# Optimization experiments

Hardware: AMD Instinct MI355X
Metric: run time of the kernel (lower is better)

The kernel has to match this reference:

```python
import jax, jax.numpy as jnp
import numpy as np

N_HEAD = 16


def setup_inputs() -> dict:
    key = jax.random.key(0)
    ks = jax.random.split(key, 4)
    B, S, E = 1, 4096, 1024
    x = jax.random.normal(ks[0], (B, S, E), dtype=jnp.float32)
    # causal mask: True where attention is DISALLOWED (upper triangle)
    masked_matrix = ~jnp.tril(jnp.ones((S, S), dtype=bool))[None, None]
    Wqkv = jax.random.normal(ks[1], (E, 3 * E), dtype=jnp.float32) * (1.0 / np.sqrt(E))
    bqkv = jnp.zeros((3 * E,), dtype=jnp.float32)
    Wp = jax.random.normal(ks[2], (E, E), dtype=jnp.float32) * (1.0 / np.sqrt(E))
    bp = jnp.zeros((E,), dtype=jnp.float32)
    return {"x": x, "masked_matrix": masked_matrix, "Wqkv": Wqkv, "bqkv": bqkv,
            "Wp": Wp, "bp": bp}


def reference(x, masked_matrix, Wqkv, bqkv, Wp, bp):
    B, S, E = x.shape
    H = N_HEAD
    D = E // H
    qkv = x @ Wqkv + bqkv                        # [B,S,3E]
    q, k, v = jnp.split(qkv, 3, axis=-1)
    q = q.reshape(B, S, H, D).transpose(0, 2, 1, 3)  # [B,H,S,D]
    k = k.reshape(B, S, H, D).transpose(0, 2, 1, 3)
    v = v.reshape(B, S, H, D).transpose(0, 2, 1, 3)
    # NOTE: source applies NO 1/sqrt(D) scaling — kept faithful.
    att = jnp.einsum('bhqd,bhkd->bhqk', q, k)    # [B,H,S,S]
    att = jnp.where(masked_matrix, jnp.float32(-jnp.inf), att)
    att = jax.nn.softmax(att, axis=-1)
    res = jnp.einsum('bhqk,bhkd->bhqd', att, v)  # [B,H,S,D]
    res = res.transpose(0, 2, 1, 3).reshape(B, S, E)
    return res @ Wp + bp
```

## Files before the change

### kernel.cpp

```cpp
#include <hip/hip_runtime.h>
#include <hip/hip_bf16.h>
#include <math.h>

#define S_LEN 4096
#define EMB   1024
#define NHEAD 16
#define HDIM  64

typedef __attribute__((ext_vector_type(8))) _Float16 half8;
typedef __attribute__((ext_vector_type(4))) _Float16 half4;
typedef __attribute__((ext_vector_type(4))) float float4_t;

#define GLOBAL_AS(p) ((const __attribute__((address_space(1))) void*)(p))
#define LDS_AS(p)    ((__attribute__((address_space(3))) void*)(p))

#define LOG2E 1.4426950408889634f

__global__ __launch_bounds__(256) void convert_f16(
    const float* __restrict__ in, _Float16* __restrict__ out)
{
    const int i = blockIdx.x * 256 + threadIdx.x;
    const float4_t v = ((const float4_t*)in)[i];
    half4 h;
#pragma unroll
    for (int j = 0; j < 4; ++j) h[j] = (_Float16)v[j];
    ((half4*)out)[i] = h;
}

__global__ __launch_bounds__(256) void transpose_f16(
    const float* __restrict__ in, _Float16* __restrict__ out, int R, int C)
{
    __shared__ float t[64][65];
    const int r0 = blockIdx.y * 64, c0 = blockIdx.x * 64;
    for (int i = threadIdx.x; i < 64 * 64; i += 256) {
        int r = i >> 6, c = i & 63;
        t[r][c] = in[(size_t)(r0 + r) * C + c0 + c];
    }
    __syncthreads();
    for (int i = threadIdx.x; i < 64 * 64; i += 256) {
        int c = i >> 6, r = i & 63;
        out[(size_t)(c0 + c) * R + r0 + r] = (_Float16)t[r][c];
    }
}

__global__ __launch_bounds__(256) void gemm_qkv(
    const _Float16* __restrict__ Ag, const _Float16* __restrict__ Bg,
    const float* __restrict__ bias,
    _Float16* __restrict__ qk, _Float16* __restrict__ vt, int K)
{
    constexpr int BK = 32;
    __shared__ _Float16 Ah[128 * BK];
    __shared__ _Float16 Bh[128 * BK];

    const int tid = threadIdx.x;
    const int wave = tid >> 6, lane = tid & 63;
    const int l16 = lane & 15, quad = lane >> 4;
    const int wr = wave >> 1, wc = wave & 1;
    const int row0 = blockIdx.y * 128, col0 = blockIdx.x * 128;
    const int lrow = lane >> 2, lc8 = (lane & 3) * 8;

    float4_t acc[4][4];
#pragma unroll
    for (int i = 0; i < 4; ++i)
#pragma unroll
        for (int j = 0; j < 4; ++j) acc[i][j] = (float4_t){0.f, 0.f, 0.f, 0.f};

    for (int k0 = 0; k0 < K; k0 += BK) {
        __syncthreads();
#pragma unroll
        for (int i = 0; i < 2; ++i) {
            const int ar = i * 64 + wave * 16;
            __builtin_amdgcn_global_load_lds(
                GLOBAL_AS(Ag + (size_t)(row0 + ar + lrow) * K + k0 + lc8),
                LDS_AS(&Ah[ar * BK]), 16, 0, 0);
            __builtin_amdgcn_global_load_lds(
                GLOBAL_AS(Bg + (size_t)(col0 + ar + lrow) * K + k0 + lc8),
                LDS_AS(&Bh[ar * BK]), 16, 0, 0);
        }
        __syncthreads();

        half8 af[4], bfr[4];
#pragma unroll
        for (int t = 0; t < 4; ++t) {
            af[t]  = *(const half8*)&Ah[(wr * 64 + t * 16 + l16) * BK + quad * 8];
            bfr[t] = *(const half8*)&Bh[(wc * 64 + t * 16 + l16) * BK + quad * 8];
        }
#pragma unroll
        for (int i = 0; i < 4; ++i)
#pragma unroll
            for (int j = 0; j < 4; ++j)
                acc[i][j] = __builtin_amdgcn_mfma_f32_16x16x32_f16(af[i], bfr[j], acc[i][j], 0, 0, 0);
    }

#pragma unroll
    for (int i = 0; i < 4; ++i) {
#pragma unroll
        for (int j = 0; j < 4; ++j) {
            const int colb = col0 + wc * 64 + j * 16 + l16;
            const float bv = bias[colb];
#pragma unroll
            for (int r = 0; r < 4; ++r) {
                const int row = row0 + wr * 64 + i * 16 + quad * 4 + r;
                float val = acc[i][j][r] + bv;
                if (colb < 2048) {
                    if (colb >= 1024) val *= LOG2E;
                    qk[(size_t)row * 2048 + colb] = (_Float16)val;
                } else {
                    vt[(size_t)(colb - 2048) * 4096 + row] = (_Float16)val;
                }
            }
        }
    }
}

__global__ __launch_bounds__(256) void gemm_out(
    const _Float16* __restrict__ Ag, const _Float16* __restrict__ Bg,
    const float* __restrict__ bias, float* __restrict__ C, int N, int K)
{
    constexpr int BK = 32;
    __shared__ _Float16 Ah[128 * BK];
    __shared__ _Float16 Bh[128 * BK];

    const int tid = threadIdx.x;
    const int wave = tid >> 6, lane = tid & 63;
    const int l16 = lane & 15, quad = lane >> 4;
    const int wr = wave >> 1, wc = wave & 1;
    const int row0 = blockIdx.y * 128, col0 = blockIdx.x * 128;
    const int lrow = lane >> 2, lc8 = (lane & 3) * 8;

    float4_t acc[4][4];
#pragma unroll
    for (int i = 0; i < 4; ++i)
#pragma unroll
        for (int j = 0; j < 4; ++j) acc[i][j] = (float4_t){0.f, 0.f, 0.f, 0.f};

    for (int k0 = 0; k0 < K; k0 += BK) {
        __syncthreads();
#pragma unroll
        for (int i = 0; i < 2; ++i) {
            const int ar = i * 64 + wave * 16;
            __builtin_amdgcn_global_load_lds(
                GLOBAL_AS(Ag + (size_t)(row0 + ar + lrow) * K + k0 + lc8),
                LDS_AS(&Ah[ar * BK]), 16, 0, 0);
            __builtin_amdgcn_global_load_lds(
                GLOBAL_AS(Bg + (size_t)(col0 + ar + lrow) * K + k0 + lc8),
                LDS_AS(&Bh[ar * BK]), 16, 0, 0);
        }
        __syncthreads();

        half8 af[4], bfr[4];
#pragma unroll
        for (int t = 0; t < 4; ++t) {
            af[t]  = *(const half8*)&Ah[(wr * 64 + t * 16 + l16) * BK + quad * 8];
            bfr[t] = *(const half8*)&Bh[(wc * 64 + t * 16 + l16) * BK + quad * 8];
        }
#pragma unroll
        for (int i = 0; i < 4; ++i)
#pragma unroll
            for (int j = 0; j < 4; ++j)
                acc[i][j] = __builtin_amdgcn_mfma_f32_16x16x32_f16(af[i], bfr[j], acc[i][j], 0, 0, 0);
    }

#pragma unroll
    for (int i = 0; i < 4; ++i) {
#pragma unroll
        for (int j = 0; j < 4; ++j) {
            const int colb = col0 + wc * 64 + j * 16 + l16;
            const float bv = bias[colb];
#pragma unroll
            for (int r = 0; r < 4; ++r) {
                const int row = row0 + wr * 64 + i * 16 + quad * 4 + r;
                C[(size_t)row * N + colb] = acc[i][j][r] + bv;
            }
        }
    }
}

__global__ __launch_bounds__(128, 2) void flash_attn_f16(
    const _Float16* __restrict__ qk, const _Float16* __restrict__ v_t,
    _Float16* __restrict__ resh)
{
    __shared__ __align__(16) _Float16 Ks[64][72];
    __shared__ __align__(16) _Float16 Vt[64][72];
    __shared__ __align__(16) _Float16 Pb[2][16][72];

    const int bid  = blockIdx.x;
    const int h    = (bid & 7) * 2 + ((bid >> 3) & 1);
    const int pair = bid >> 4;
    const int tid  = threadIdx.x;
    const int wave = tid >> 6;
    const int lane = tid & 63;
    const int l16  = lane & 15;
    const int quad = lane >> 4;
    const int srow = tid >> 3;
    const int sc8  = (tid & 7) * 8;

    for (int half = 0; half < 2; ++half) {
        const int tile = half ? 127 - pair : pair;
        const int q0   = tile * 32 + wave * 16;
        const int kb_last = (tile >> 1) * 64;

        const size_t qoff = (size_t)(q0 + l16) * 2048 + h * HDIM + quad * 8;
        half8 qf0 = *(const half8*)(qk + qoff);
        half8 qf1 = *(const half8*)(qk + qoff + 32);

        float4_t o[4];
#pragma unroll
        for (int c = 0; c < 4; ++c) o[c] = (float4_t){0.f, 0.f, 0.f, 0.f};
        float m_r = -INFINITY, l_r = 0.f;

        half8 pf_k[4], pf_v[4];
#pragma unroll
        for (int p = 0; p < 4; ++p) {
            const int r = srow + p * 16;
            pf_k[p] = *(const half8*)(qk + (size_t)r * 2048 + 1024 + h * HDIM + sc8);
            pf_v[p] = *(const half8*)(v_t + (size_t)(h * HDIM + r) * 4096 + sc8);
        }

        for (int kb = 0; kb <= kb_last; kb += 64) {
            __syncthreads();
#pragma unroll
            for (int p = 0; p < 4; ++p) {
                const int r = srow + p * 16;
                *(half8*)&Ks[r][sc8] = pf_k[p];
                *(half8*)&Vt[r][sc8] = pf_v[p];
            }
            __syncthreads();

            if (kb < kb_last) {
                const int kn = kb + 64;
#pragma unroll
                for (int p = 0; p < 4; ++p) {
                    const int r = srow + p * 16;
                    pf_k[p] = *(const half8*)(qk + (size_t)(kn + r) * 2048 + 1024 + h * HDIM + sc8);
                    pf_v[p] = *(const half8*)(v_t + (size_t)(h * HDIM + r) * 4096 + kn + sc8);
                }
            }

            if (kb > q0 + 15) continue;

            float4_t s[4];
#pragma unroll
            for (int t = 0; t < 4; ++t) {
                half8 a0 = *(const half8*)&Ks[t * 16 + l16][quad * 8];
                half8 a1 = *(const half8*)&Ks[t * 16 + l16][32 + quad * 8];
                float4_t a = (float4_t){0.f, 0.f, 0.f, 0.f};
                a = __builtin_amdgcn_mfma_f32_16x16x32_f16(a0, qf0, a, 0, 0, 0);
                a = __builtin_amdgcn_mfma_f32_16x16x32_f16(a1, qf1, a, 0, 0, 0);
                s[t] = a;
            }

            if (kb + 63 > q0) {
                const int qg = q0 + l16;
#pragma unroll
                for (int t = 0; t < 4; ++t)
#pragma unroll
                    for (int r = 0; r < 4; ++r) {
                        const int key = kb + t * 16 + quad * 4 + r;
                        if (key > qg) s[t][r] = -INFINITY;
                    }
            }

            float mx = s[0][0];
#pragma unroll
            for (int t = 0; t < 4; ++t)
#pragma unroll
                for (int r = 0; r < 4; ++r) mx = fmaxf(mx, s[t][r]);
            mx = fmaxf(mx, __shfl_xor(mx, 16));
            mx = fmaxf(mx, __shfl_xor(mx, 32));
            const float mnew  = fmaxf(m_r, mx);
            const float alpha = __builtin_amdgcn_exp2f(m_r - mnew);

            float p[4][4];
            float sum = 0.f;
#pragma unroll
            for (int t = 0; t < 4; ++t)
#pragma unroll
                for (int r = 0; r < 4; ++r) {
                    p[t][r] = __builtin_amdgcn_exp2f(s[t][r] - mnew);
                    sum += p[t][r];
                }
            sum += __shfl_xor(sum, 16);
            sum += __shfl_xor(sum, 32);
            l_r = l_r * alpha + sum;
            m_r = mnew;
#pragma unroll
            for (int ct = 0; ct < 4; ++ct)
#pragma unroll
                for (int r = 0; r < 4; ++r) o[ct][r] *= alpha;

#pragma unroll
            for (int t = 0; t < 4; ++t) {
                half4 w;
#pragma unroll
                for (int r = 0; r < 4; ++r) w[r] = (_Float16)p[t][r];
                *(half4*)&Pb[wave][l16][t * 16 + quad * 4] = w;
            }
            half8 pb0 = *(const half8*)&Pb[wave][l16][quad * 8];
            half8 pb1 = *(const half8*)&Pb[wave][l16][32 + quad * 8];

#pragma unroll
            for (int ct = 0; ct < 4; ++ct) {
                half8 va0 = *(const half8*)&Vt[ct * 16 + l16][quad * 8];
                half8 va1 = *(const half8*)&Vt[ct * 16 + l16][32 + quad * 8];
                o[ct] = __builtin_amdgcn_mfma_f32_16x16x32_f16(va0, pb0, o[ct], 0, 0, 0);
                o[ct] = __builtin_amdgcn_mfma_f32_16x16x32_f16(va1, pb1, o[ct], 0, 0, 0);
            }
        }

        const float inv = 1.0f / l_r;
#pragma unroll
        for (int ct = 0; ct < 4; ++ct) {
            half4 w;
#pragma unroll
            for (int r = 0; r < 4; ++r) w[r] = (_Float16)(o[ct][r] * inv);
            *(half4*)&resh[(size_t)(q0 + l16) * EMB + h * HDIM + ct * 16 + quad * 4] = w;
        }
    }
}

extern "C" void kernel_launch(void* const* d_in, const int* in_sizes, int n_in,
                              void* d_out, int out_size, void* d_ws, size_t ws_size,
                              hipStream_t stream)
{
    const float* x    = (const float*)d_in[0];
    const float* Wqkv = (const float*)d_in[2];
    const float* bqkv = (const float*)d_in[3];
    const float* Wp   = (const float*)d_in[4];
    const float* bp   = (const float*)d_in[5];
    float* out = (float*)d_out;

    _Float16* xh  = (_Float16*)d_ws;
    _Float16* WTh = xh + (size_t)4096 * 1024;
    _Float16* qkh = WTh + (size_t)3072 * 1024;
    _Float16* vtg = qkh + (size_t)4096 * 2048;
    _Float16* resh = xh;
    _Float16* WpT  = WTh;

    dim3 blk(256);

    convert_f16<<<4096, blk, 0, stream>>>(x, xh);
    transpose_f16<<<dim3(3072 / 64, 1024 / 64), blk, 0, stream>>>(
        Wqkv, WTh, 1024, 3072);

    gemm_qkv<<<dim3(3072 / 128, 4096 / 128), blk, 0, stream>>>(
        xh, WTh, bqkv, qkh, vtg, 1024);

    transpose_f16<<<dim3(1024 / 64, 1024 / 64), blk, 0, stream>>>(
        Wp, WpT, 1024, 1024);

    flash_attn_f16<<<dim3(1024), dim3(128), 0, stream>>>(qkh, vtg, resh);

    gemm_out<<<dim3(1024 / 128, 4096 / 128), blk, 0, stream>>>(
        resh, WpT, bp, out, 1024, 1024);
}
```

Baseline: 287.0 us.

## Merge prep kernels, vectorize V stores, make flash-attn waves independent

Three launches (x conversion and both weight transposes) become one prep kernel, with WpT given its own workspace region. The gemm_qkv V-transpose stores now write half4 vectors instead of scalars. The attention kernel gives each wave its own 16-query tile and private K tile in LDS, removing the block-wide __syncthreads, and V fragments are read directly from global memory into registers instead of through LDS. This trades barrier stalls and LDS traffic for redundant global K/V reads per wave and more register pressure.

Result: slower. 330.4 us (+15.1%).

```diff
diff --git a/kernel.cpp b/kernel.cpp
--- a/kernel.cpp
+++ b/kernel.cpp
@@ -16,22 +16,36 @@
 
 #define LOG2E 1.4426950408889634f
 
-__global__ __launch_bounds__(256) void convert_f16(
-    const float* __restrict__ in, _Float16* __restrict__ out)
-{
-    const int i = blockIdx.x * 256 + threadIdx.x;
-    const float4_t v = ((const float4_t*)in)[i];
-    half4 h;
-#pragma unroll
-    for (int j = 0; j < 4; ++j) h[j] = (_Float16)v[j];
-    ((half4*)out)[i] = h;
-}
-
-__global__ __launch_bounds__(256) void transpose_f16(
-    const float* __restrict__ in, _Float16* __restrict__ out, int R, int C)
-{
+__global__ __launch_bounds__(256) void prep(
+    const float* __restrict__ x, const float* __restrict__ Wqkv,
+    const float* __restrict__ Wp,
+    _Float16* __restrict__ xh, _Float16* __restrict__ WTh,
+    _Float16* __restrict__ WpT)
+{
+    const int bid = blockIdx.x;
+    if (bid < 4096) {
+        const int i = bid * 256 + threadIdx.x;
+        const float4_t v = ((const float4_t*)x)[i];
+        half4 hh;
+#pragma unroll
+        for (int j = 0; j < 4; ++j) hh[j] = (_Float16)v[j];
+        ((half4*)xh)[i] = hh;
+        return;
+    }
     __shared__ float t[64][65];
-    const int r0 = blockIdx.y * 64, c0 = blockIdx.x * 64;
+    const float* in;
+    _Float16* out;
+    int R, C, bx, by;
+    if (bid < 4096 + 768) {
+        const int idx = bid - 4096;
+        bx = idx % 48; by = idx / 48;
+        in = Wqkv; out = WTh; R = 1024; C = 3072;
+    } else {
+        const int idx = bid - 4864;
+        bx = idx & 15; by = idx >> 4;
+        in = Wp; out = WpT; R = 1024; C = 1024;
+    }
+    const int r0 = by * 64, c0 = bx * 64;
     for (int i = threadIdx.x; i < 64 * 64; i += 256) {
         int r = i >> 6, c = i & 63;
         t[r][c] = in[(size_t)(r0 + r) * C + c0 + c];
@@ -98,16 +112,18 @@
         for (int j = 0; j < 4; ++j) {
             const int colb = col0 + wc * 64 + j * 16 + l16;
             const float bv = bias[colb];
-#pragma unroll
-            for (int r = 0; r < 4; ++r) {
-                const int row = row0 + wr * 64 + i * 16 + quad * 4 + r;
-                float val = acc[i][j][r] + bv;
-                if (colb < 2048) {
-                    if (colb >= 1024) val *= LOG2E;
-                    qk[(size_t)row * 2048 + colb] = (_Float16)val;
-                } else {
-                    vt[(size_t)(colb - 2048) * 4096 + row] = (_Float16)val;
-                }
+            const int rowb = row0 + wr * 64 + i * 16 + quad * 4;
+            if (colb < 2048) {
+                const float sc = (colb >= 1024) ? LOG2E : 1.0f;
+#pragma unroll
+                for (int r = 0; r < 4; ++r)
+                    qk[(size_t)(rowb + r) * 2048 + colb] =
+                        (_Float16)((acc[i][j][r] + bv) * sc);
+            } else {
+                half4 w;
+#pragma unroll
+                for (int r = 0; r < 4; ++r) w[r] = (_Float16)(acc[i][j][r] + bv);
+                *(half4*)&vt[(size_t)(colb - 2048) * 4096 + rowb] = w;
             }
         }
     }
@@ -180,25 +196,26 @@
     const _Float16* __restrict__ qk, const _Float16* __restrict__ v_t,
     _Float16* __restrict__ resh)
 {
-    __shared__ __align__(16) _Float16 Ks[64][72];
-    __shared__ __align__(16) _Float16 Vt[64][72];
+    __shared__ __align__(16) _Float16 Ks[2][64][72];
     __shared__ __align__(16) _Float16 Pb[2][16][72];
 
     const int bid  = blockIdx.x;
     const int h    = (bid & 7) * 2 + ((bid >> 3) & 1);
-    const int pair = bid >> 4;
-    const int tid  = threadIdx.x;
-    const int wave = tid >> 6;
-    const int lane = tid & 63;
+    const int wave = threadIdx.x >> 6;
+    const int lane = threadIdx.x & 63;
     const int l16  = lane & 15;
     const int quad = lane >> 4;
-    const int srow = tid >> 3;
-    const int sc8  = (tid & 7) * 8;
+    const int pw   = (bid >> 4) * 2 + wave;
+    const int srow = lane >> 3;
+    const int sc8  = (lane & 7) * 8;
+
+    const _Float16* kplane = qk + 1024 + h * HDIM;
+    const _Float16* vplane = v_t + (size_t)h * HDIM * 4096;
 
     for (int half = 0; half < 2; ++half) {
-        const int tile = half ? 127 - pair : pair;
-        const int q0   = tile * 32 + wave * 16;
-        const int kb_last = (tile >> 1) * 64;
+        const int tile = half ? 255 - pw : pw;
+        const int q0   = tile * 16;
+        const int kb_last = (tile >> 2) * 64;
 
         const size_t qoff = (size_t)(q0 + l16) * 2048 + h * HDIM + quad * 8;
         half8 qf0 = *(const half8*)(qk + qoff);
@@ -209,41 +226,36 @@
         for (int c = 0; c < 4; ++c) o[c] = (float4_t){0.f, 0.f, 0.f, 0.f};
         float m_r = -INFINITY, l_r = 0.f;
 
-        half8 pf_k[4], pf_v[4];
-#pragma unroll
-        for (int p = 0; p < 4; ++p) {
-            const int r = srow + p * 16;
-            pf_k[p] = *(const half8*)(qk + (size_t)r * 2048 + 1024 + h * HDIM + sc8);
-            pf_v[p] = *(const half8*)(v_t + (size_t)(h * HDIM + r) * 4096 + sc8);
-        }
+        half8 pf_k[8];
+#pragma unroll
+        for (int p = 0; p < 8; ++p)
+            pf_k[p] = *(const half8*)(kplane + (size_t)(srow + p * 8) * 2048 + sc8);
 
         for (int kb = 0; kb <= kb_last; kb += 64) {
-            __syncthreads();
-#pragma unroll
-            for (int p = 0; p < 4; ++p) {
-                const int r = srow + p * 16;
-                *(half8*)&Ks[r][sc8] = pf_k[p];
-                *(half8*)&Vt[r][sc8] = pf_v[p];
-            }
-            __syncthreads();
+#pragma unroll
+            for (int p = 0; p < 8; ++p)
+                *(half8*)&Ks[wave][srow + p * 8][sc8] = pf_k[p];
 
             if (kb < kb_last) {
                 const int kn = kb + 64;
 #pragma unroll
-                for (int p = 0; p < 4; ++p) {
-                    const int r = srow + p * 16;
-                    pf_k[p] = *(const half8*)(qk + (size_t)(kn + r) * 2048 + 1024 + h * HDIM + sc8);
-                    pf_v[p] = *(const half8*)(v_t + (size_t)(h * HDIM + r) * 4096 + kn + sc8);
-                }
-            }
-
-            if (kb > q0 + 15) continue;
+                for (int p = 0; p < 8; ++p)
+                    pf_k[p] = *(const half8*)(kplane + (size_t)(kn + srow + p * 8) * 2048 + sc8);
+            }
+
+            half8 va0[4], va1[4];
+#pragma unroll
+            for (int ct = 0; ct < 4; ++ct) {
+                const _Float16* vp = vplane + (size_t)(ct * 16 + l16) * 4096 + kb + quad * 8;
+                va0[ct] = *(const half8*)(vp);
+                va1[ct] = *(const half8*)(vp + 32);
+            }
 
             float4_t s[4];
 #pragma unroll
             for (int t = 0; t < 4; ++t) {
-                half8 a0 = *(const half8*)&Ks[t * 16 + l16][quad * 8];
-                half8 a1 = *(const half8*)&Ks[t * 16 + l16][32 + quad * 8];
+                half8 a0 = *(const half8*)&Ks[wave][t * 16 + l16][quad * 8];
+                half8 a1 = *(const half8*)&Ks[wave][t * 16 + l16][32 + quad * 8];
                 float4_t a = (float4_t){0.f, 0.f, 0.f, 0.f};
                 a = __builtin_amdgcn_mfma_f32_16x16x32_f16(a0, qf0, a, 0, 0, 0);
                 a = __builtin_amdgcn_mfma_f32_16x16x32_f16(a1, qf1, a, 0, 0, 0);
@@ -301,10 +313,8 @@
 
 #pragma unroll
             for (int ct = 0; ct < 4; ++ct) {
-                half8 va0 = *(const half8*)&Vt[ct * 16 + l16][quad * 8];
-                half8 va1 = *(const half8*)&Vt[ct * 16 + l16][32 + quad * 8];
-                o[ct] = __builtin_amdgcn_mfma_f32_16x16x32_f16(va0, pb0, o[ct], 0, 0, 0);
-                o[ct] = __builtin_amdgcn_mfma_f32_16x16x32_f16(va1, pb1, o[ct], 0, 0, 0);
+                o[ct] = __builtin_amdgcn_mfma_f32_16x16x32_f16(va0[ct], pb0, o[ct], 0, 0, 0);
+                o[ct] = __builtin_amdgcn_mfma_f32_16x16x32_f16(va1[ct], pb1, o[ct], 0, 0, 0);
             }
         }
 
@@ -334,21 +344,16 @@
     _Float16* WTh = xh + (size_t)4096 * 1024;
     _Float16* qkh = WTh + (size_t)3072 * 1024;
     _Float16* vtg = qkh + (size_t)4096 * 2048;
+    _Float16* WpT = vtg + (size_t)1024 * 4096;
     _Float16* resh = xh;
-    _Float16* WpT  = WTh;
 
     dim3 blk(256);
 
-    convert_f16<<<4096, blk, 0, stream>>>(x, xh);
-    transpose_f16<<<dim3(3072 / 64, 1024 / 64), blk, 0, stream>>>(
-        Wqkv, WTh, 1024, 3072);
+    prep<<<dim3(5120), blk, 0, stream>>>(x, Wqkv, Wp, xh, WTh, WpT);
 
     gemm_qkv<<<dim3(3072 / 128, 4096 / 128), blk, 0, stream>>>(
         xh, WTh, bqkv, qkh, vtg, 1024);
 
-    transpose_f16<<<dim3(1024 / 64, 1024 / 64), blk, 0, stream>>>(
-        Wp, WpT, 1024, 1024);
-
     flash_attn_f16<<<dim3(1024), dim3(128), 0, stream>>>(qkh, vtg, resh);
 
     gemm_out<<<dim3(1024 / 128, 4096 / 128), blk, 0, stream>>>(
```
